# Optimization experiments

Measured on AMD Instinct MI355X. Metric: run time of the kernel, lower is better.

Reference implementation:

```python
import jax, jax.numpy as jnp
import numpy as np

N, D, C = 8192, 128, 64
LAMBDA = 0.25
DELTA = 1.0


def setup_inputs() -> dict:
    key = jax.random.key(0)
    k1, k2, k3 = jax.random.split(key, 3)
    out = jax.random.normal(k1, (N, C), dtype=jnp.float32)
    feat = jax.random.normal(k2, (N, D), dtype=jnp.float32)
    y = jax.random.randint(k3, (N,), 0, C)
    return {"out": out, "feat": feat, "y": y}


def reference(out, feat, y):
    n = feat.shape[0]
    # Per-class matrices: zeroing rows not in class c leaves singular values
    # identical to slicing X[y==c] (extra zero rows only add zero singular
    # directions), so one batched SVD over [C, N, D] replaces the CPU loop.
    masks = (y[None, :] == jnp.arange(C)[:, None]).astype(feat.dtype)  # [C, N]
    Xc = feat[None, :, :] * masks[:, :, None]                           # [C, N, D]
    Sc = jnp.linalg.svd(Xc, compute_uv=False)                           # [C, min(N,D)]
    obj_c = jnp.maximum(Sc.sum(-1), DELTA).sum()                        # sum_c max(||X_c||_*, DELTA)
    S_all = jnp.linalg.svd(feat, compute_uv=False)
    ole = (obj_c - S_all.sum()) / n * LAMBDA
    # Cross entropy (mean reduction, matching nn.CrossEntropyLoss)
    logp = jax.nn.log_softmax(out, axis=-1)
    xe = -jnp.take_along_axis(logp, y[:, None], axis=1).mean()
    loss = ole + xe
    return jnp.reshape(loss, (1,))  # torch returns shape-[1] tensor
```

## Files before the change

kernel.cpp:

```cpp
#include <hip/hip_runtime.h>
#include <math.h>


#define N_ROWS 8192
#define DIM    128
#define NCLS   64
#define NMAT   65
#define NITER  7
#define EPSN   2e-4f
#define LAMBDA_ 0.25f
#define DELTA_  1.0f
#define MAGIC  0x13579BDF

typedef __attribute__((ext_vector_type(8))) short s16x8;
typedef __attribute__((ext_vector_type(4))) short s16x4;
typedef __attribute__((ext_vector_type(4))) float f32x4;

static __device__ const float NS_C1[NITER] =
  {2.554408f, 2.491084f, 2.189178f, 2.050122f, 1.686417f, 1.5f, 1.5f};
static __device__ const float NS_C2[NITER] =
  {2.469261f, 2.290137f, 1.554316f, 1.276543f, 0.710544f, 0.5f, 0.5f};

__device__ __forceinline__ unsigned short f2bf(float f) {
  unsigned u = __float_as_uint(f);
  u = (u + 0x7FFFu + ((u >> 16) & 1u)) >> 16;
  return (unsigned short)u;
}
__device__ __forceinline__ float bf2f(unsigned short h) {
  return __uint_as_float(((unsigned)h) << 16);
}

__device__ __forceinline__ int swz_idx(int i, int j) {
  return i * 128 + (((j >> 3) ^ (i & 15)) << 3) + (j & 7);
}

__device__ __forceinline__ s16x8 load_frag(const short* buf, int row0,
                                           int kstep, int lane) {
  int m  = row0 + (lane & 15);
  int kg = kstep * 4 + (lane >> 4);
  return *(const s16x8*)(buf + m * 128 + ((kg ^ (m & 15)) << 3));
}

__device__ __forceinline__ void flag_set(int* p) {
  __threadfence();
  __hip_atomic_store(p, MAGIC, __ATOMIC_RELEASE, __HIP_MEMORY_SCOPE_AGENT);
}
__device__ __forceinline__ void flag_wait(const int* p) {
  while (__hip_atomic_load(p, __ATOMIC_ACQUIRE, __HIP_MEMORY_SCOPE_AGENT) != MAGIC)
    __builtin_amdgcn_s_sleep(8);
}

__global__ __launch_bounds__(256) void ole_gram_ce(const float* __restrict__ feat,
                                                   const int* __restrict__ y,
                                                   const float* __restrict__ logits,
                                                   float* __restrict__ G,
                                                   float* __restrict__ cepart) {
  __shared__ int   list[N_ROWS];
  __shared__ int   cnt;
  __shared__ float xs[8][DIM];

  const int tid = threadIdx.x;

  if (blockIdx.x >= NCLS) {
    const int blk    = blockIdx.x - NCLS;
    const int gwave  = blk * 4 + (tid >> 6);
    const int lane   = tid & 63;

    float acc = 0.f;
    for (int row = gwave; row < N_ROWS; row += 512) {
      float v = logits[row * NCLS + lane];
      float mx = v;
      for (int off = 32; off > 0; off >>= 1) mx = fmaxf(mx, __shfl_xor(mx, off, 64));
      float e = expf(v - mx);
      for (int off = 32; off > 0; off >>= 1) e += __shfl_xor(e, off, 64);
      if (lane == 0) {
        int t = y[row];
        acc += (mx + logf(e)) - logits[row * NCLS + t];
      }
    }
    if (lane == 0) cepart[gwave] = acc;
    return;
  }

  const int c  = blockIdx.x;
  const int ti = tid >> 4, tj = tid & 15;
  const int i0 = ti * 8,  j0 = tj * 8;

  if (tid == 0) cnt = 0;
  __syncthreads();
  const int4* y4 = (const int4*)y;
#pragma unroll
  for (int t = 0; t < 8; ++t) {
    int g4 = tid + 256 * t;
    int4 v = y4[g4];
    int r0 = g4 * 4;
    if (v.x == c) list[atomicAdd(&cnt, 1)] = r0;
    if (v.y == c) list[atomicAdd(&cnt, 1)] = r0 + 1;
    if (v.z == c) list[atomicAdd(&cnt, 1)] = r0 + 2;
    if (v.w == c) list[atomicAdd(&cnt, 1)] = r0 + 3;
  }
  __syncthreads();
  const int n = cnt;

  float acc[8][8];
#pragma unroll
  for (int a = 0; a < 8; ++a)
#pragma unroll
    for (int b = 0; b < 8; ++b) acc[a][b] = 0.f;

  const int ldrow = tid >> 5;
  const int ldcol = (tid & 31) * 4;

  for (int base = 0; base < n; base += 8) {
    __syncthreads();
    int li = base + ldrow;
    float4 v = make_float4(0.f, 0.f, 0.f, 0.f);
    if (li < n) v = *(const float4*)(feat + (size_t)list[li] * DIM + ldcol);
    *(float4*)(&xs[ldrow][ldcol]) = v;
    __syncthreads();
#pragma unroll
    for (int rw = 0; rw < 8; ++rw) {
      float xi[8], xj[8];
#pragma unroll
      for (int a = 0; a < 8; ++a) xi[a] = xs[rw][i0 + a];
#pragma unroll
      for (int b = 0; b < 8; ++b) xj[b] = xs[rw][j0 + b];
#pragma unroll
      for (int a = 0; a < 8; ++a)
#pragma unroll
        for (int b = 0; b < 8; ++b) acc[a][b] = fmaf(xi[a], xj[b], acc[a][b]);
    }
  }

  float* Gc = G + (size_t)c * DIM * DIM;
#pragma unroll
  for (int a = 0; a < 8; ++a)
#pragma unroll
    for (int b = 0; b < 8; ++b)
      Gc[(i0 + a) * DIM + (j0 + b)] = acc[a][b];
}

__global__ __launch_bounds__(512, 1) void ole_ns(const float* __restrict__ G,
                                                 float* __restrict__ Gmut,
                                                 float* __restrict__ nuc,
                                                 const float* __restrict__ cepart,
                                                 int* __restrict__ gallf,
                                                 int* __restrict__ nflag,
                                                 float* __restrict__ out) {
  __shared__ short Yb[DIM * DIM];
  __shared__ short Mh[DIM * DIM];
  __shared__ short Ml[DIM * DIM];
  __shared__ short Zb[DIM * DIM];

  const int bid  = blockIdx.x;
  const int tid  = threadIdx.x;
  const int lane = tid & 63;
  const int quad = lane >> 4;
  const int wv   = tid >> 6;

  if (bid > NCLS) {
    const int gb = bid - NCLS - 1;
    if (tid < 256) {
      int idx4 = gb * 256 + tid;
      const float4* G4 = (const float4*)G;
      float4 s = make_float4(0.f, 0.f, 0.f, 0.f);
#pragma unroll 8
      for (int c = 0; c < NCLS; ++c) {
        float4 v = G4[(size_t)c * (DIM * DIM / 4) + idx4];
        s.x += v.x; s.y += v.y; s.z += v.z; s.w += v.w;
      }
      ((float4*)Gmut)[(size_t)NCLS * (DIM * DIM / 4) + idx4] = s;
    }
    __syncthreads();
    if (tid == 0) flag_set(&gallf[gb]);
    return;
  }

  if (bid == NCLS) {
    if (tid < 16) flag_wait(&gallf[tid]);
    __syncthreads();
  }

  const int wr = wv >> 2;
  const int wc = wv & 3;

  const float4* Gm4 = (const float4*)(G + (size_t)bid * DIM * DIM);

  float4 gs[8];
  float tpart = 0.f, fpart = 0.f;
#pragma unroll
  for (int t = 0; t < 8; ++t) {
    int idx4 = tid + 512 * t;
    float4 v = Gm4[idx4];
    gs[t] = v;
    fpart += v.x * v.x + v.y * v.y + v.z * v.z + v.w * v.w;
    int flat = idx4 * 4, i = flat >> 7, j0 = flat & 127;
    if (j0 <= i && i < j0 + 4) tpart += ((const float*)&v)[i - j0];
  }
  for (int off = 32; off > 0; off >>= 1) {
    tpart += __shfl_down(tpart, off, 64);
    fpart += __shfl_down(fpart, off, 64);
  }
  float* redf = (float*)Zb;
  if (lane == 0) { redf[wv] = tpart; redf[8 + wv] = fpart; }
  __syncthreads();
  float trace = 0.f, fro2 = 0.f;
#pragma unroll
  for (int w = 0; w < 8; ++w) { trace += redf[w]; fro2 += redf[8 + w]; }
  __syncthreads();

  float s = sqrtf(fro2);
  if (s < 1e-12f) s = 1.f;
  const float invs = 1.f / s;
  const float eps  = EPSN * trace * invs;

#pragma unroll
  for (int t = 0; t < 8; ++t) {
    int idx4 = tid + 512 * t;
    int flat = idx4 * 4, i = flat >> 7, j0 = flat & 127;
    s16x4 vh;
#pragma unroll
    for (int e = 0; e < 4; ++e) {
      float x = ((const float*)&gs[t])[e] * invs + ((i == j0 + e) ? eps : 0.f);
      vh[e] = (short)f2bf(x);
    }
    *(s16x4*)(Yb + swz_idx(i, j0)) = vh;
  }
  for (int grp = tid; grp < DIM * 16; grp += 512) {
    int i = grp >> 4, g = grp & 15;
    s16x8 v = (s16x8)0;
    if ((i >> 3) == g) v[i & 7] = (short)0x3F80;
    *(s16x8*)(Zb + i * 128 + ((g ^ (i & 15)) << 3)) = v;
  }
  __syncthreads();

  for (int it = 0; it < NITER; ++it) {
    const float kA = NS_C1[it];
    const float kB = NS_C2[it];

    f32x4 acc[4][2];
#pragma unroll
    for (int r = 0; r < 4; ++r)
#pragma unroll
      for (int c2 = 0; c2 < 2; ++c2) acc[r][c2] = (f32x4)0.f;
#pragma unroll
    for (int ks = 0; ks < 4; ++ks) {
      s16x8 a[4], b[2];
#pragma unroll
      for (int r = 0; r < 4; ++r) a[r] = load_frag(Zb, (4 * wr + r) * 16, ks, lane);
#pragma unroll
      for (int c2 = 0; c2 < 2; ++c2) b[c2] = load_frag(Yb, (2 * wc + c2) * 16, ks, lane);
#pragma unroll
      for (int r = 0; r < 4; ++r)
#pragma unroll
        for (int c2 = 0; c2 < 2; ++c2)
          acc[r][c2] = __builtin_amdgcn_mfma_f32_16x16x32_bf16(a[r], b[c2], acc[r][c2], 0, 0, 0);
    }
#pragma unroll
    for (int r = 0; r < 4; ++r) {
      int ibase = (4 * wr + r) * 16 + quad * 4;
      int cg    = ibase >> 3;
#pragma unroll
      for (int c2 = 0; c2 < 2; ++c2) {
        int jg  = (2 * wc + c2) * 16 + (lane & 15);
        int idx = jg * 128 + ((cg ^ (jg & 15)) << 3) + (ibase & 7);
        s16x4 vh, vl;
#pragma unroll
        for (int e = 0; e < 4; ++e) {
          float mv = -kB * acc[r][c2][e] + ((ibase + e == jg) ? kA : 0.f);
          mv = fminf(fmaxf(mv, -4.f), 4.f);
          unsigned short hh = f2bf(mv);
          vh[e] = (short)hh;
          vl[e] = (short)f2bf(mv - bf2f(hh));
        }
        *(s16x4*)(Mh + idx) = vh;
        *(s16x4*)(Ml + idx) = vl;
      }
    }
    __syncthreads();

    f32x4 ay[4][2], az[4][2];
#pragma unroll
    for (int r = 0; r < 4; ++r)
#pragma unroll
      for (int c2 = 0; c2 < 2; ++c2) { ay[r][c2] = (f32x4)0.f; az[r][c2] = (f32x4)0.f; }
#pragma unroll
    for (int ks = 0; ks < 4; ++ks) {
      s16x8 aMh[4], aMl[4], bY[2], bZ[2];
#pragma unroll
      for (int r = 0; r < 4; ++r) {
        int rb = (4 * wr + r) * 16;
        aMh[r] = load_frag(Mh, rb, ks, lane);
        aMl[r] = load_frag(Ml, rb, ks, lane);
      }
#pragma unroll
      for (int c2 = 0; c2 < 2; ++c2) {
        int cb = (2 * wc + c2) * 16;
        bY[c2] = load_frag(Yb, cb, ks, lane);
        bZ[c2] = load_frag(Zb, cb, ks, lane);
      }
#pragma unroll
      for (int r = 0; r < 4; ++r)
#pragma unroll
        for (int c2 = 0; c2 < 2; ++c2) {
          ay[r][c2] = __builtin_amdgcn_mfma_f32_16x16x32_bf16(aMh[r], bY[c2], ay[r][c2], 0, 0, 0);
          ay[r][c2] = __builtin_amdgcn_mfma_f32_16x16x32_bf16(aMl[r], bY[c2], ay[r][c2], 0, 0, 0);
          az[r][c2] = __builtin_amdgcn_mfma_f32_16x16x32_bf16(aMh[r], bZ[c2], az[r][c2], 0, 0, 0);
          az[r][c2] = __builtin_amdgcn_mfma_f32_16x16x32_bf16(aMl[r], bZ[c2], az[r][c2], 0, 0, 0);
        }
    }
    __syncthreads();

#pragma unroll
    for (int r = 0; r < 4; ++r) {
      int ibase = (4 * wr + r) * 16 + quad * 4;
      int cg    = ibase >> 3;
#pragma unroll
      for (int c2 = 0; c2 < 2; ++c2) {
        int jg  = (2 * wc + c2) * 16 + (lane & 15);
        int idx = jg * 128 + ((cg ^ (jg & 15)) << 3) + (ibase & 7);
        s16x4 vy, vz;
#pragma unroll
        for (int e = 0; e < 4; ++e) {
          vy[e] = (short)f2bf(ay[r][c2][e]);
          vz[e] = (short)f2bf(az[r][c2][e]);
        }
        *(s16x4*)(Yb + idx) = vy;
        *(s16x4*)(Zb + idx) = vz;
      }
    }
    __syncthreads();
  }

  float t_gz = 0.f, t_z = 0.f, t_z3 = 0.f;
#pragma unroll
  for (int t = 0; t < 8; ++t) {
    int idx4 = tid + 512 * t;
    int flat = idx4 * 4, i = flat >> 7, j0 = flat & 127;
    s16x4 zv = *(const s16x4*)(Zb + swz_idx(i, j0));
#pragma unroll
    for (int e = 0; e < 4; ++e) t_gz += ((const float*)&gs[t])[e] * bf2f((unsigned short)zv[e]);
  }
  if (tid < DIM) t_z = bf2f((unsigned short)Zb[swz_idx(tid, tid)]);

  {
    f32x4 u[4][2];
#pragma unroll
    for (int r = 0; r < 4; ++r)
#pragma unroll
      for (int c2 = 0; c2 < 2; ++c2) u[r][c2] = (f32x4)0.f;
#pragma unroll
    for (int ks = 0; ks < 4; ++ks) {
      s16x8 a[4], b[2];
#pragma unroll
      for (int r = 0; r < 4; ++r) a[r] = load_frag(Zb, (4 * wr + r) * 16, ks, lane);
#pragma unroll
      for (int c2 = 0; c2 < 2; ++c2) b[c2] = load_frag(Zb, (2 * wc + c2) * 16, ks, lane);
#pragma unroll
      for (int r = 0; r < 4; ++r)
#pragma unroll
        for (int c2 = 0; c2 < 2; ++c2)
          u[r][c2] = __builtin_amdgcn_mfma_f32_16x16x32_bf16(a[r], b[c2], u[r][c2], 0, 0, 0);
    }
#pragma unroll
    for (int r = 0; r < 4; ++r) {
      int ibase = (4 * wr + r) * 16 + quad * 4;
      int cg    = ibase >> 3;
#pragma unroll
      for (int c2 = 0; c2 < 2; ++c2) {
        int jg  = (2 * wc + c2) * 16 + (lane & 15);
        int idx = jg * 128 + ((cg ^ (jg & 15)) << 3) + (ibase & 7);
        s16x4 zt = *(const s16x4*)(Zb + idx);
#pragma unroll
        for (int e = 0; e < 4; ++e) t_z3 += u[r][c2][e] * bf2f((unsigned short)zt[e]);
      }
    }
  }

  for (int off = 32; off > 0; off >>= 1) {
    t_gz += __shfl_down(t_gz, off, 64);
    t_z  += __shfl_down(t_z,  off, 64);
    t_z3 += __shfl_down(t_z3, off, 64);
  }
  __syncthreads();
  float* red = (float*)Mh;
  if (lane == 0) { red[wv] = t_gz; red[8 + wv] = t_z; red[16 + wv] = t_z3; }
  __syncthreads();

  float nuc_own = 0.f;
  if (tid == 0) {
    float gz = 0.f, z1 = 0.f, z3 = 0.f;
#pragma unroll
    for (int w = 0; w < 8; ++w) { gz += red[w]; z1 += red[8 + w]; z3 += red[16 + w]; }
    float trsq = gz * invs + 0.5f * eps * z1 - 0.125f * eps * eps * z3;
    nuc_own = sqrtf(s) * trsq;
    nuc[bid] = nuc_own;
  }

  if (bid < NCLS) {
    if (tid == 0) flag_set(&nflag[bid]);
    return;
  }

  if (tid < NCLS) flag_wait(&nflag[tid]);
  __syncthreads();

  float ce2 = cepart[tid];
  float vmx = (tid < NCLS) ? fmaxf(nuc[tid], DELTA_) : 0.f;
  for (int off = 32; off > 0; off >>= 1) {
    vmx += __shfl_down(vmx, off, 64);
    ce2 += __shfl_down(ce2, off, 64);
  }
  if (lane == 0) { red[wv] = vmx; red[8 + wv] = ce2; }
  __syncthreads();
  if (tid == 0) {
    float vs = 0.f, cs = 0.f;
#pragma unroll
    for (int w = 0; w < 8; ++w) { vs += red[w]; cs += red[8 + w]; }
    float ole = (vs - nuc_own) * (LAMBDA_ / (float)N_ROWS);
    out[0] = ole + cs / (float)N_ROWS;
  }
}

extern "C" void kernel_launch(void* const* d_in, const int* in_sizes, int n_in,
                              void* d_out, int out_size, void* d_ws, size_t ws_size,
                              hipStream_t stream) {
  const float* logits = (const float*)d_in[0];
  const float* feat   = (const float*)d_in[1];
  const int*   yp     = (const int*)d_in[2];

  float* G      = (float*)d_ws;
  float* nuc    = G + (size_t)NMAT * DIM * DIM;
  float* cepart = nuc + NMAT + 3;
  int*   gallf  = (int*)(cepart + 512);
  int*   nflag  = gallf + 16;

  ole_gram_ce<<<NCLS + 128, 256, 0, stream>>>(feat, yp, logits, G, cepart);
  ole_ns<<<NMAT + 16, 512, 0, stream>>>(G, G, nuc, cepart, gallf, nflag,
                                        (float*)d_out);
}
```

Measured before the change: 140.3 us.

## Fuse Gram, cross-entropy and Newton-Schulz into one kernel with flag sync

Merges the per-class Gram kernel and the Newton-Schulz kernel into a single launch. Each class block builds its Gram matrix in registers, feeds it straight into its own iteration without a global round trip, and atomically adds it into a shared full-data Gram. The full-matrix block waits on per-class flags, and the cross-entropy blocks signal completion through flags as well. This removes one kernel launch, the per-class Gram storage and the separate summation pass. In exchange it adds a memset, 8192×64 float atomics, and a spin-wait that relies on all 129 blocks being resident at the same time.

```diff
diff --git a/kernel.cpp b/kernel.cpp
--- a/kernel.cpp
+++ b/kernel.cpp
@@ -5,7 +5,6 @@
 #define N_ROWS 8192
 #define DIM    128
 #define NCLS   64
-#define NMAT   65
 #define NITER  7
 #define EPSN   2e-4f
 #define LAMBDA_ 0.25f
@@ -50,22 +49,32 @@
     __builtin_amdgcn_s_sleep(8);
 }
 
-__global__ __launch_bounds__(256) void ole_gram_ce(const float* __restrict__ feat,
-                                                   const int* __restrict__ y,
-                                                   const float* __restrict__ logits,
-                                                   float* __restrict__ G,
-                                                   float* __restrict__ cepart) {
-  __shared__ int   list[N_ROWS];
-  __shared__ int   cnt;
-  __shared__ float xs[8][DIM];
-
-  const int tid = threadIdx.x;
-
-  if (blockIdx.x >= NCLS) {
-    const int blk    = blockIdx.x - NCLS;
-    const int gwave  = blk * 4 + (tid >> 6);
-    const int lane   = tid & 63;
-
+__global__ __launch_bounds__(512, 1) void ole_fused(const float* __restrict__ feat,
+                                                    const int* __restrict__ y,
+                                                    const float* __restrict__ logits,
+                                                    float* __restrict__ Gall,
+                                                    float* __restrict__ nuc,
+                                                    float* __restrict__ cepart,
+                                                    int* __restrict__ flags,
+                                                    float* __restrict__ out) {
+  int* gramdone = flags;
+  int* nflag    = flags + NCLS;
+  int* ceflag   = flags + 2 * NCLS;
+
+  __shared__ __align__(16) short Yb[DIM * DIM];
+  __shared__ __align__(16) short Mh[DIM * DIM];
+  __shared__ __align__(16) short Ml[DIM * DIM];
+  __shared__ __align__(16) short Zb[DIM * DIM];
+  __shared__ int cnt;
+
+  const int bid  = blockIdx.x;
+  const int tid  = threadIdx.x;
+  const int lane = tid & 63;
+  const int quad = lane >> 4;
+  const int wv   = tid >> 6;
+
+  if (bid > NCLS) {
+    const int gwave = (bid - NCLS - 1) * 8 + wv;
     float acc = 0.f;
     for (int row = gwave; row < N_ROWS; row += 512) {
       float v = logits[row * NCLS + lane];
@@ -79,124 +88,90 @@
       }
     }
     if (lane == 0) cepart[gwave] = acc;
+    __syncthreads();
+    if (tid == 0) flag_set(&ceflag[bid - NCLS - 1]);
     return;
   }
 
-  const int c  = blockIdx.x;
-  const int ti = tid >> 4, tj = tid & 15;
-  const int i0 = ti * 8,  j0 = tj * 8;
-
-  if (tid == 0) cnt = 0;
-  __syncthreads();
-  const int4* y4 = (const int4*)y;
-#pragma unroll
-  for (int t = 0; t < 8; ++t) {
-    int g4 = tid + 256 * t;
-    int4 v = y4[g4];
-    int r0 = g4 * 4;
-    if (v.x == c) list[atomicAdd(&cnt, 1)] = r0;
-    if (v.y == c) list[atomicAdd(&cnt, 1)] = r0 + 1;
-    if (v.z == c) list[atomicAdd(&cnt, 1)] = r0 + 2;
-    if (v.w == c) list[atomicAdd(&cnt, 1)] = r0 + 3;
-  }
-  __syncthreads();
-  const int n = cnt;
-
-  float acc[8][8];
-#pragma unroll
-  for (int a = 0; a < 8; ++a)
-#pragma unroll
-    for (int b = 0; b < 8; ++b) acc[a][b] = 0.f;
-
-  const int ldrow = tid >> 5;
-  const int ldcol = (tid & 31) * 4;
-
-  for (int base = 0; base < n; base += 8) {
-    __syncthreads();
-    int li = base + ldrow;
-    float4 v = make_float4(0.f, 0.f, 0.f, 0.f);
-    if (li < n) v = *(const float4*)(feat + (size_t)list[li] * DIM + ldcol);
-    *(float4*)(&xs[ldrow][ldcol]) = v;
-    __syncthreads();
-#pragma unroll
-    for (int rw = 0; rw < 8; ++rw) {
-      float xi[8], xj[8];
-#pragma unroll
-      for (int a = 0; a < 8; ++a) xi[a] = xs[rw][i0 + a];
-#pragma unroll
-      for (int b = 0; b < 8; ++b) xj[b] = xs[rw][j0 + b];
-#pragma unroll
-      for (int a = 0; a < 8; ++a)
-#pragma unroll
-        for (int b = 0; b < 8; ++b) acc[a][b] = fmaf(xi[a], xj[b], acc[a][b]);
-    }
-  }
-
-  float* Gc = G + (size_t)c * DIM * DIM;
-#pragma unroll
-  for (int a = 0; a < 8; ++a)
-#pragma unroll
-    for (int b = 0; b < 8; ++b)
-      Gc[(i0 + a) * DIM + (j0 + b)] = acc[a][b];
-}
-
-__global__ __launch_bounds__(512, 1) void ole_ns(const float* __restrict__ G,
-                                                 float* __restrict__ Gmut,
-                                                 float* __restrict__ nuc,
-                                                 const float* __restrict__ cepart,
-                                                 int* __restrict__ gallf,
-                                                 int* __restrict__ nflag,
-                                                 float* __restrict__ out) {
-  __shared__ short Yb[DIM * DIM];
-  __shared__ short Mh[DIM * DIM];
-  __shared__ short Ml[DIM * DIM];
-  __shared__ short Zb[DIM * DIM];
-
-  const int bid  = blockIdx.x;
-  const int tid  = threadIdx.x;
-  const int lane = tid & 63;
-  const int quad = lane >> 4;
-  const int wv   = tid >> 6;
-
-  if (bid > NCLS) {
-    const int gb = bid - NCLS - 1;
-    if (tid < 256) {
-      int idx4 = gb * 256 + tid;
-      const float4* G4 = (const float4*)G;
-      float4 s = make_float4(0.f, 0.f, 0.f, 0.f);
-#pragma unroll 8
-      for (int c = 0; c < NCLS; ++c) {
-        float4 v = G4[(size_t)c * (DIM * DIM / 4) + idx4];
-        s.x += v.x; s.y += v.y; s.z += v.z; s.w += v.w;
-      }
-      ((float4*)Gmut)[(size_t)NCLS * (DIM * DIM / 4) + idx4] = s;
-    }
-    __syncthreads();
-    if (tid == 0) flag_set(&gallf[gb]);
-    return;
-  }
-
-  if (bid == NCLS) {
-    if (tid < 16) flag_wait(&gallf[tid]);
-    __syncthreads();
-  }
-
-  const int wr = wv >> 2;
-  const int wc = wv & 3;
-
-  const float4* Gm4 = (const float4*)(G + (size_t)bid * DIM * DIM);
-
+  const int ti = tid >> 5, tj = tid & 31;
+  const int i0 = ti * 8,  j0 = tj * 4;
+
+  float  accg[8][4];
   float4 gs[8];
   float tpart = 0.f, fpart = 0.f;
-#pragma unroll
-  for (int t = 0; t < 8; ++t) {
-    int idx4 = tid + 512 * t;
-    float4 v = Gm4[idx4];
-    gs[t] = v;
-    fpart += v.x * v.x + v.y * v.y + v.z * v.z + v.w * v.w;
-    int flat = idx4 * 4, i = flat >> 7, j0 = flat & 127;
-    if (j0 <= i && i < j0 + 4) tpart += ((const float*)&v)[i - j0];
-  }
+
+  if (bid < NCLS) {
+    int* list = (int*)Yb;
+    float (*xs)[DIM] = (float (*)[DIM])Mh;
+
+    if (tid == 0) cnt = 0;
+    __syncthreads();
+    const int4* y4 = (const int4*)y;
+#pragma unroll
+    for (int t = 0; t < 4; ++t) {
+      int g4 = tid + 512 * t;
+      int4 v = y4[g4];
+      int r0 = g4 * 4;
+      if (v.x == bid) list[atomicAdd(&cnt, 1)] = r0;
+      if (v.y == bid) list[atomicAdd(&cnt, 1)] = r0 + 1;
+      if (v.z == bid) list[atomicAdd(&cnt, 1)] = r0 + 2;
+      if (v.w == bid) list[atomicAdd(&cnt, 1)] = r0 + 3;
+    }
+    __syncthreads();
+    const int n = cnt;
+
+#pragma unroll
+    for (int a = 0; a < 8; ++a)
+#pragma unroll
+      for (int b = 0; b < 4; ++b) accg[a][b] = 0.f;
+
+    for (int base = 0; base < n; base += 16) {
+      int li = base + ti;
+      float4 v = make_float4(0.f, 0.f, 0.f, 0.f);
+      if (li < n) v = *(const float4*)(feat + (size_t)list[li] * DIM + j0);
+      __syncthreads();
+      *(float4*)(&xs[ti][j0]) = v;
+      __syncthreads();
+#pragma unroll
+      for (int rw = 0; rw < 16; ++rw) {
+        float xi[8], xj[4];
+#pragma unroll
+        for (int a = 0; a < 8; ++a) xi[a] = xs[rw][i0 + a];
+#pragma unroll
+        for (int b = 0; b < 4; ++b) xj[b] = xs[rw][j0 + b];
+#pragma unroll
+        for (int a = 0; a < 8; ++a)
+#pragma unroll
+          for (int b = 0; b < 4; ++b) accg[a][b] = fmaf(xi[a], xj[b], accg[a][b]);
+      }
+    }
+
+#pragma unroll
+    for (int a = 0; a < 8; ++a)
+#pragma unroll
+      for (int b = 0; b < 4; ++b) {
+        float g = accg[a][b];
+        atomicAdd(&Gall[(i0 + a) * DIM + (j0 + b)], g);
+        fpart += g * g;
+        if (i0 + a == j0 + b) tpart += g;
+      }
+    __syncthreads();
+    if (tid == 0) flag_set(&gramdone[bid]);
+  } else {
+    if (tid < NCLS) flag_wait(&gramdone[tid]);
+    __syncthreads();
+    const float4* Gm4 = (const float4*)Gall;
+#pragma unroll
+    for (int t = 0; t < 8; ++t) {
+      int idx4 = tid + 512 * t;
+      float4 v = Gm4[idx4];
+      gs[t] = v;
+      fpart += v.x * v.x + v.y * v.y + v.z * v.z + v.w * v.w;
+      int flat = idx4 * 4, i = flat >> 7, jj = flat & 127;
+      if (jj <= i && i < jj + 4) tpart += ((const float*)&v)[i - jj];
+    }
+  }
+
   for (int off = 32; off > 0; off >>= 1) {
     tpart += __shfl_down(tpart, off, 64);
     fpart += __shfl_down(fpart, off, 64);
@@ -214,17 +189,31 @@
   const float invs = 1.f / s;
   const float eps  = EPSN * trace * invs;
 
-#pragma unroll
-  for (int t = 0; t < 8; ++t) {
-    int idx4 = tid + 512 * t;
-    int flat = idx4 * 4, i = flat >> 7, j0 = flat & 127;
-    s16x4 vh;
-#pragma unroll
-    for (int e = 0; e < 4; ++e) {
-      float x = ((const float*)&gs[t])[e] * invs + ((i == j0 + e) ? eps : 0.f);
-      vh[e] = (short)f2bf(x);
-    }
-    *(s16x4*)(Yb + swz_idx(i, j0)) = vh;
+  if (bid < NCLS) {
+#pragma unroll
+    for (int a = 0; a < 8; ++a) {
+      int i = i0 + a;
+      s16x4 vh;
+#pragma unroll
+      for (int b = 0; b < 4; ++b) {
+        float x = accg[a][b] * invs + ((i == j0 + b) ? eps : 0.f);
+        vh[b] = (short)f2bf(x);
+      }
+      *(s16x4*)(Yb + swz_idx(i, j0)) = vh;
+    }
+  } else {
+#pragma unroll
+    for (int t = 0; t < 8; ++t) {
+      int idx4 = tid + 512 * t;
+      int flat = idx4 * 4, i = flat >> 7, jj = flat & 127;
+      s16x4 vh;
+#pragma unroll
+      for (int e = 0; e < 4; ++e) {
+        float x = ((const float*)&gs[t])[e] * invs + ((i == jj + e) ? eps : 0.f);
+        vh[e] = (short)f2bf(x);
+      }
+      *(s16x4*)(Yb + swz_idx(i, jj)) = vh;
+    }
   }
   for (int grp = tid; grp < DIM * 16; grp += 512) {
     int i = grp >> 4, g = grp & 15;
@@ -233,6 +222,9 @@
     *(s16x8*)(Zb + i * 128 + ((g ^ (i & 15)) << 3)) = v;
   }
   __syncthreads();
+
+  const int wr = wv >> 2;
+  const int wc = wv & 3;
 
   for (int it = 0; it < NITER; ++it) {
     const float kA = NS_C1[it];
@@ -333,13 +325,22 @@
   }
 
   float t_gz = 0.f, t_z = 0.f, t_z3 = 0.f;
-#pragma unroll
-  for (int t = 0; t < 8; ++t) {
-    int idx4 = tid + 512 * t;
-    int flat = idx4 * 4, i = flat >> 7, j0 = flat & 127;
-    s16x4 zv = *(const s16x4*)(Zb + swz_idx(i, j0));
-#pragma unroll
-    for (int e = 0; e < 4; ++e) t_gz += ((const float*)&gs[t])[e] * bf2f((unsigned short)zv[e]);
+  if (bid < NCLS) {
+#pragma unroll
+    for (int a = 0; a < 8; ++a) {
+      s16x4 zv = *(const s16x4*)(Zb + swz_idx(i0 + a, j0));
+#pragma unroll
+      for (int b = 0; b < 4; ++b) t_gz += accg[a][b] * bf2f((unsigned short)zv[b]);
+    }
+  } else {
+#pragma unroll
+    for (int t = 0; t < 8; ++t) {
+      int idx4 = tid + 512 * t;
+      int flat = idx4 * 4, i = flat >> 7, jj = flat & 127;
+      s16x4 zv = *(const s16x4*)(Zb + swz_idx(i, jj));
+#pragma unroll
+      for (int e = 0; e < 4; ++e) t_gz += ((const float*)&gs[t])[e] * bf2f((unsigned short)zv[e]);
+    }
   }
   if (tid < DIM) t_z = bf2f((unsigned short)Zb[swz_idx(tid, tid)]);
 
@@ -402,7 +403,8 @@
     return;
   }
 
-  if (tid < NCLS) flag_wait(&nflag[tid]);
+  if (tid < NCLS)          flag_wait(&nflag[tid]);
+  else if (tid < 2 * NCLS) flag_wait(&ceflag[tid - NCLS]);
   __syncthreads();
 
   float ce2 = cepart[tid];
@@ -429,13 +431,13 @@
   const float* feat   = (const float*)d_in[1];
   const int*   yp     = (const int*)d_in[2];
 
-  float* G      = (float*)d_ws;
-  float* nuc    = G + (size_t)NMAT * DIM * DIM;
-  float* cepart = nuc + NMAT + 3;
-  int*   gallf  = (int*)(cepart + 512);
-  int*   nflag  = gallf + 16;
-
-  ole_gram_ce<<<NCLS + 128, 256, 0, stream>>>(feat, yp, logits, G, cepart);
-  ole_ns<<<NMAT + 16, 512, 0, stream>>>(G, G, nuc, cepart, gallf, nflag,
-                                        (float*)d_out);
-}
+  float* Gall   = (float*)d_ws;
+  int*   flags  = (int*)(Gall + DIM * DIM);
+  float* nuc    = (float*)(flags + 192);
+  float* cepart = nuc + 68;
+
+  hipMemsetAsync(d_ws, 0, (DIM * DIM + 192) * sizeof(float), stream);
+
+  ole_fused<<<2 * NCLS + 1, 512, 0, stream>>>(feat, yp, logits, Gall, nuc,
+                                              cepart, flags, (float*)d_out);
+}
```

New measurement: 132.8 us. 1.06x faster.
